# Optimization experiments

Measured on AMD Instinct MI355X. Metric: run time of the kernel, lower is better.

The kernel has to match this reference:

```python
import jax, jax.numpy as jnp
import numpy as np

B, T, D, U = 64, 4096, 256, 64

def setup_inputs() -> dict:
    key = jax.random.key(0)
    k1, k2, k3 = jax.random.split(key, 3)
    inputs = jax.random.normal(k1, (B, T, D), dtype=jnp.float32)
    # glorot_uniform init for W (D,U) and u (U,1); zeros bias
    limW = float(np.sqrt(6.0 / (D + U)))
    W = jax.random.uniform(k2, (D, U), minval=-limW, maxval=limW, dtype=jnp.float32)
    limu = float(np.sqrt(6.0 / (U + 1)))
    u = jax.random.uniform(k3, (U, 1), minval=-limu, maxval=limu, dtype=jnp.float32)
    b = jnp.zeros((U,), dtype=jnp.float32)
    return {"inputs": inputs, "W": W, "b": b, "u": u}

def reference(inputs, W, b, u):
    # score: [B,T,U] = tanh(inputs @ W + b)
    score = jnp.tanh(jnp.einsum('btd,du->btu', inputs, W) + b)
    # logits: [B,T,1]; softmax over time axis (axis=1)
    logits = jnp.einsum('btu,uo->bto', score, u)
    attention_weights = jax.nn.softmax(logits, axis=1)
    # weighted sum over time -> [B,D]
    context = jnp.sum(inputs * attention_weights, axis=1)
    return (context, attention_weights)
```

## Files before the change

### kernel.cpp

```cpp
#include <hip/hip_runtime.h>
#include <math.h>

#define B_ 64
#define T_ 4096
#define D_ 256
#define U_ 64
#define RPB 64
#define NPB (T_ / RPB)
#define NSTRIP (RPB / 16)
#define XPAD 264

typedef float f32x4 __attribute__((ext_vector_type(4)));
typedef short bf16x8 __attribute__((ext_vector_type(8)));

__device__ __forceinline__ unsigned short f2bf_rne(float f) {
    unsigned u = __float_as_uint(f);
    unsigned r = u + 0x7fffu + ((u >> 16) & 1u);
    return (unsigned short)(r >> 16);
}
__device__ __forceinline__ float bfbits2f(unsigned short s) {
    return __uint_as_float(((unsigned)s) << 16);
}

__global__ __launch_bounds__(256) void wprep_kernel(
    const float* __restrict__ W, unsigned short* __restrict__ whi,
    unsigned short* __restrict__ wlo)
{
    int fi = blockIdx.x * 256 + threadIdx.x;
    int j    = fi & 7;
    int lane = (fi >> 3) & 63;
    int tile = fi >> 9;
    int nt = tile & 3, ks = tile >> 2;
    int k = ks * 32 + (lane >> 4) * 8 + j;
    int n = nt * 16 + (lane & 15);
    float w = W[k * U_ + n];
    unsigned short hi = f2bf_rne(w);
    unsigned short lo = f2bf_rne(w - bfbits2f(hi));
    whi[fi] = hi;
    wlo[fi] = lo;
}

__global__ __launch_bounds__(256, 4) void fused_main(
    const float* __restrict__ x, const unsigned short* __restrict__ whi,
    const unsigned short* __restrict__ wlo, const float* __restrict__ bias,
    const float* __restrict__ uvec, float* __restrict__ wts,
    float* __restrict__ Zp, float* __restrict__ Pp)
{
    __shared__ unsigned short Xh[RPB * XPAD];
    __shared__ float part[RPB][4];
    __shared__ float esh[RPB];

    int tid = threadIdx.x;
    int lane = tid & 63, wid = tid >> 6;
    int q = lane >> 4, r = lane & 15;

    bf16x8 Bh[8], Bl[8];
    {
        const bf16x8* whiV = (const bf16x8*)whi;
        const bf16x8* wloV = (const bf16x8*)wlo;
#pragma unroll
        for (int ks = 0; ks < 8; ++ks) {
            Bh[ks] = whiV[(ks * 4 + wid) * 64 + lane];
            Bl[ks] = wloV[(ks * 4 + wid) * 64 + lane];
        }
    }

    int b = blockIdx.x / NPB;
    int pb = blockIdx.x % NPB;
    size_t row00 = (size_t)b * T_ + (size_t)pb * RPB;

    int col = wid * 16 + r;
    float bv = bias[col], uv = uvec[col];

    const float* xrow = x + (row00 + r) * D_ + q * 8;

#pragma unroll 1
    for (int s = 0; s < NSTRIP; ++s) {
        const float* xp = xrow + (size_t)s * 16 * D_;
        f32x4 acc = (f32x4){0.f, 0.f, 0.f, 0.f};

#pragma unroll
        for (int h = 0; h < 2; ++h) {
            float4 xb[8];
#pragma unroll
            for (int k2 = 0; k2 < 4; ++k2) {
                xb[2 * k2]     = *(const float4*)(xp + (h * 4 + k2) * 32);
                xb[2 * k2 + 1] = *(const float4*)(xp + (h * 4 + k2) * 32 + 4);
            }
#pragma unroll
            for (int k2 = 0; k2 < 4; ++k2) {
                int ks = h * 4 + k2;
                float4 va = xb[2 * k2], vb = xb[2 * k2 + 1];
                float f[8] = {va.x, va.y, va.z, va.w, vb.x, vb.y, vb.z, vb.w};
                union { bf16x8 v; unsigned short sh[8]; uint4 u; } hi_, lo_;
#pragma unroll
                for (int j = 0; j < 8; ++j) {
                    unsigned short a = f2bf_rne(f[j]);
                    hi_.sh[j] = a;
                    lo_.sh[j] = f2bf_rne(f[j] - bfbits2f(a));
                }
                if (wid == 0)
                    *(uint4*)(&Xh[(s * 16 + r) * XPAD + ks * 32 + q * 8]) = hi_.u;
                acc = __builtin_amdgcn_mfma_f32_16x16x32_bf16(hi_.v, Bh[ks], acc, 0, 0, 0);
                acc = __builtin_amdgcn_mfma_f32_16x16x32_bf16(hi_.v, Bl[ks], acc, 0, 0, 0);
                acc = __builtin_amdgcn_mfma_f32_16x16x32_bf16(lo_.v, Bh[ks], acc, 0, 0, 0);
            }
        }

        float p0 = fmaf(1.f - 2.f / (__expf(2.f * (acc[0] + bv)) + 1.f), uv, 0.f);
        float p1 = fmaf(1.f - 2.f / (__expf(2.f * (acc[1] + bv)) + 1.f), uv, 0.f);
        float p2 = fmaf(1.f - 2.f / (__expf(2.f * (acc[2] + bv)) + 1.f), uv, 0.f);
        float p3 = fmaf(1.f - 2.f / (__expf(2.f * (acc[3] + bv)) + 1.f), uv, 0.f);
#pragma unroll
        for (int off = 1; off < 16; off <<= 1) {
            p0 += __shfl_xor(p0, off, 64);
            p1 += __shfl_xor(p1, off, 64);
            p2 += __shfl_xor(p2, off, 64);
            p3 += __shfl_xor(p3, off, 64);
        }
        if (r == 0) {
            int row = s * 16 + q * 4;
            part[row + 0][wid] = p0;
            part[row + 1][wid] = p1;
            part[row + 2][wid] = p2;
            part[row + 3][wid] = p3;
        }
    }
    __syncthreads();

    if (wid == 0) {
        float lg = (part[lane][0] + part[lane][1]) + (part[lane][2] + part[lane][3]);
        float e = __expf(lg);
        esh[lane] = e;
        wts[row00 + lane] = e;
        float z = e;
#pragma unroll
        for (int off = 1; off < 64; off <<= 1) z += __shfl_xor(z, off, 64);
        if (lane == 0) Zp[blockIdx.x] = z;
    }
    __syncthreads();

    int colg = tid & 31, ph = tid >> 5;
    float pacc[8];
#pragma unroll
    for (int j = 0; j < 8; ++j) pacc[j] = 0.f;
#pragma unroll 2
    for (int i = 0; i < RPB; i += 8) {
        int row = i + ph;
        float w = esh[row];
        union { uint4 u; unsigned short sh[8]; } v;
        v.u = *(const uint4*)(&Xh[row * XPAD + colg * 8]);
#pragma unroll
        for (int j = 0; j < 8; ++j)
            pacc[j] = fmaf(w, bfbits2f(v.sh[j]), pacc[j]);
    }
    __syncthreads();
    float* red = (float*)Xh;
#pragma unroll
    for (int j = 0; j < 8; ++j) red[ph * 256 + colg * 8 + j] = pacc[j];
    __syncthreads();
    float ssum = 0.f;
#pragma unroll
    for (int p = 0; p < 8; ++p) ssum += red[p * 256 + tid];
    Pp[(size_t)blockIdx.x * D_ + tid] = ssum;
}

__global__ __launch_bounds__(256) void finalize_kernel(
    float* __restrict__ wts, const float* __restrict__ Zp,
    const float* __restrict__ Pp, float* __restrict__ ctx)
{
    int b = blockIdx.x;
    int tid = threadIdx.x;
    float Z = 0.f;
#pragma unroll 8
    for (int i = 0; i < NPB; ++i) Z += Zp[b * NPB + i];
    float invZ = 1.f / Z;

    float s = 0.f;
#pragma unroll 4
    for (int i = 0; i < NPB; ++i) s += Pp[(size_t)(b * NPB + i) * D_ + tid];
    ctx[b * D_ + tid] = s * invZ;

    float4* wp = (float4*)(wts + (size_t)b * T_);
#pragma unroll
    for (int i = 0; i < T_ / 4 / 256; ++i) {
        float4 v = wp[tid + i * 256];
        v.x *= invZ; v.y *= invZ; v.z *= invZ; v.w *= invZ;
        wp[tid + i * 256] = v;
    }
}

extern "C" void kernel_launch(void* const* d_in, const int* in_sizes, int n_in,
                              void* d_out, int out_size, void* d_ws, size_t ws_size,
                              hipStream_t stream) {
    const float* x    = (const float*)d_in[0];
    const float* W    = (const float*)d_in[1];
    const float* bias = (const float*)d_in[2];
    const float* uvec = (const float*)d_in[3];

    float* out = (float*)d_out;
    float* ctx = out;
    float* wts = out + B_ * D_;

    unsigned short* whi = (unsigned short*)d_ws;
    unsigned short* wlo = whi + D_ * U_;
    float* Zp = (float*)(wlo + D_ * U_);
    float* Pp = Zp + B_ * NPB;

    wprep_kernel<<<D_ * U_ / 256, 256, 0, stream>>>(W, whi, wlo);
    fused_main<<<(B_ * T_) / RPB, 256, 0, stream>>>(x, whi, wlo, bias, uvec, wts, Zp, Pp);
    finalize_kernel<<<B_, 256, 0, stream>>>(wts, Zp, Pp, ctx);
}
```

Before: 411.0 us.

## Stage x tile once in LDS as bf16 hi/lo and halve rows per block

Before, each of the four waves loaded the same x rows from global memory and split them into bf16 hi/lo itself, so the conversion and global reads were repeated four times per block. Now the block loads its x tile once with coalesced float4 reads, converts it cooperatively into shared hi/lo arrays, and every wave reads its MFMA operands from LDS. Rows per block drop from 64 to 32, which doubles the block count and the number of partial sums the finalize kernel has to reduce. The extra LDS array raises shared memory use per block and adds a barrier before the matrix multiply.

```diff
diff --git a/kernel.cpp b/kernel.cpp
--- a/kernel.cpp
+++ b/kernel.cpp
@@ -5,9 +5,8 @@
 #define T_ 4096
 #define D_ 256
 #define U_ 64
-#define RPB 64
+#define RPB 32
 #define NPB (T_ / RPB)
-#define NSTRIP (RPB / 16)
 #define XPAD 264
 
 typedef float f32x4 __attribute__((ext_vector_type(4)));
@@ -46,7 +45,8 @@
     const float* __restrict__ uvec, float* __restrict__ wts,
     float* __restrict__ Zp, float* __restrict__ Pp)
 {
-    __shared__ unsigned short Xh[RPB * XPAD];
+    __shared__ unsigned short Ahi[RPB * XPAD];
+    __shared__ unsigned short Alo[RPB * XPAD];
     __shared__ float part[RPB][4];
     __shared__ float esh[RPB];
 
@@ -69,44 +69,48 @@
     int pb = blockIdx.x % NPB;
     size_t row00 = (size_t)b * T_ + (size_t)pb * RPB;
 
+    {
+        const float4* xs4 = (const float4*)(x + row00 * D_);
+        float4 xs[8];
+#pragma unroll
+        for (int i = 0; i < 8; ++i) xs[i] = xs4[tid + i * 256];
+#pragma unroll
+        for (int i = 0; i < 8; ++i) {
+            int f = tid + i * 256;
+            int row = f >> 6, c4 = f & 63;
+            float4 v = xs[i];
+            unsigned short h0 = f2bf_rne(v.x), h1 = f2bf_rne(v.y),
+                           h2 = f2bf_rne(v.z), h3 = f2bf_rne(v.w);
+            unsigned short l0 = f2bf_rne(v.x - bfbits2f(h0)),
+                           l1 = f2bf_rne(v.y - bfbits2f(h1)),
+                           l2 = f2bf_rne(v.z - bfbits2f(h2)),
+                           l3 = f2bf_rne(v.w - bfbits2f(h3));
+            int base = row * XPAD + c4 * 4;
+            uint2 hp = { (unsigned)h0 | ((unsigned)h1 << 16),
+                         (unsigned)h2 | ((unsigned)h3 << 16) };
+            uint2 lp = { (unsigned)l0 | ((unsigned)l1 << 16),
+                         (unsigned)l2 | ((unsigned)l3 << 16) };
+            *(uint2*)(&Ahi[base]) = hp;
+            *(uint2*)(&Alo[base]) = lp;
+        }
+    }
+    __syncthreads();
+
     int col = wid * 16 + r;
     float bv = bias[col], uv = uvec[col];
 
-    const float* xrow = x + (row00 + r) * D_ + q * 8;
-
-#pragma unroll 1
-    for (int s = 0; s < NSTRIP; ++s) {
-        const float* xp = xrow + (size_t)s * 16 * D_;
+#pragma unroll
+    for (int s = 0; s < 2; ++s) {
         f32x4 acc = (f32x4){0.f, 0.f, 0.f, 0.f};
-
-#pragma unroll
-        for (int h = 0; h < 2; ++h) {
-            float4 xb[8];
-#pragma unroll
-            for (int k2 = 0; k2 < 4; ++k2) {
-                xb[2 * k2]     = *(const float4*)(xp + (h * 4 + k2) * 32);
-                xb[2 * k2 + 1] = *(const float4*)(xp + (h * 4 + k2) * 32 + 4);
-            }
-#pragma unroll
-            for (int k2 = 0; k2 < 4; ++k2) {
-                int ks = h * 4 + k2;
-                float4 va = xb[2 * k2], vb = xb[2 * k2 + 1];
-                float f[8] = {va.x, va.y, va.z, va.w, vb.x, vb.y, vb.z, vb.w};
-                union { bf16x8 v; unsigned short sh[8]; uint4 u; } hi_, lo_;
-#pragma unroll
-                for (int j = 0; j < 8; ++j) {
-                    unsigned short a = f2bf_rne(f[j]);
-                    hi_.sh[j] = a;
-                    lo_.sh[j] = f2bf_rne(f[j] - bfbits2f(a));
-                }
-                if (wid == 0)
-                    *(uint4*)(&Xh[(s * 16 + r) * XPAD + ks * 32 + q * 8]) = hi_.u;
-                acc = __builtin_amdgcn_mfma_f32_16x16x32_bf16(hi_.v, Bh[ks], acc, 0, 0, 0);
-                acc = __builtin_amdgcn_mfma_f32_16x16x32_bf16(hi_.v, Bl[ks], acc, 0, 0, 0);
-                acc = __builtin_amdgcn_mfma_f32_16x16x32_bf16(lo_.v, Bh[ks], acc, 0, 0, 0);
-            }
-        }
-
+        int arow = (s * 16 + r) * XPAD + q * 8;
+#pragma unroll
+        for (int ks = 0; ks < 8; ++ks) {
+            bf16x8 ahi = *(const bf16x8*)(&Ahi[arow + ks * 32]);
+            bf16x8 alo = *(const bf16x8*)(&Alo[arow + ks * 32]);
+            acc = __builtin_amdgcn_mfma_f32_16x16x32_bf16(ahi, Bh[ks], acc, 0, 0, 0);
+            acc = __builtin_amdgcn_mfma_f32_16x16x32_bf16(ahi, Bl[ks], acc, 0, 0, 0);
+            acc = __builtin_amdgcn_mfma_f32_16x16x32_bf16(alo, Bh[ks], acc, 0, 0, 0);
+        }
         float p0 = fmaf(1.f - 2.f / (__expf(2.f * (acc[0] + bv)) + 1.f), uv, 0.f);
         float p1 = fmaf(1.f - 2.f / (__expf(2.f * (acc[1] + bv)) + 1.f), uv, 0.f);
         float p2 = fmaf(1.f - 2.f / (__expf(2.f * (acc[2] + bv)) + 1.f), uv, 0.f);
@@ -128,14 +132,14 @@
     }
     __syncthreads();
 
-    if (wid == 0) {
+    if (wid == 0 && lane < RPB) {
         float lg = (part[lane][0] + part[lane][1]) + (part[lane][2] + part[lane][3]);
         float e = __expf(lg);
         esh[lane] = e;
         wts[row00 + lane] = e;
         float z = e;
 #pragma unroll
-        for (int off = 1; off < 64; off <<= 1) z += __shfl_xor(z, off, 64);
+        for (int off = 1; off < 32; off <<= 1) z += __shfl_xor(z, off, 32);
         if (lane == 0) Zp[blockIdx.x] = z;
     }
     __syncthreads();
@@ -144,18 +148,18 @@
     float pacc[8];
 #pragma unroll
     for (int j = 0; j < 8; ++j) pacc[j] = 0.f;
-#pragma unroll 2
+#pragma unroll
     for (int i = 0; i < RPB; i += 8) {
         int row = i + ph;
         float w = esh[row];
         union { uint4 u; unsigned short sh[8]; } v;
-        v.u = *(const uint4*)(&Xh[row * XPAD + colg * 8]);
+        v.u = *(const uint4*)(&Ahi[row * XPAD + colg * 8]);
 #pragma unroll
         for (int j = 0; j < 8; ++j)
             pacc[j] = fmaf(w, bfbits2f(v.sh[j]), pacc[j]);
     }
     __syncthreads();
-    float* red = (float*)Xh;
+    float* red = (float*)Alo;
 #pragma unroll
     for (int j = 0; j < 8; ++j) red[ph * 256 + colg * 8 + j] = pacc[j];
     __syncthreads();
```

New measurement: 370.9 us. 1.11x faster.
